# Kernel tuning notes

Hardware: AMD Instinct MI355X
Metric: run time of the kernel (lower is better)

The kernel has to match this reference:

```python
import jax, jax.numpy as jnp
import numpy as np

NV = 10           # int(0.5 // 0.05), clamped to [2, 1000]
STEP = 0.05
HALF_V = 0.5
EPS = 1e-8


def _normalize(x):
    return x / (jnp.linalg.norm(x, axis=-1, keepdims=True) + EPS)


def _bilinear(img, uv):
    # img: [3, H, W]; uv: [N, 2] normalized to [0, 1). align_corners=False convention.
    C, H, W = img.shape
    x = uv[:, 0] * W - 0.5
    y = uv[:, 1] * H - 0.5
    x0 = jnp.floor(x); y0 = jnp.floor(y)
    wx = x - x0; wy = y - y0
    x0i = jnp.clip(x0.astype(jnp.int32), 0, W - 1)
    x1i = jnp.clip(x0i + 1, 0, W - 1)
    y0i = jnp.clip(y0.astype(jnp.int32), 0, H - 1)
    y1i = jnp.clip(y0i + 1, 0, H - 1)
    g = lambda yi, xi: img[:, yi, xi].T  # [N, 3]
    return (g(y0i, x0i) * ((1 - wx) * (1 - wy))[:, None]
            + g(y0i, x1i) * (wx * (1 - wy))[:, None]
            + g(y1i, x0i) * ((1 - wx) * wy)[:, None]
            + g(y1i, x1i) * (wx * wy)[:, None])


def _forward(edge_points, rgb1, rgb2, intrinsic1, intrinsic2, extrinsic1, extrinsic2, nh):
    # nh: concrete numpy int64 [E] of per-edge horizontal sample counts (non-differentiable).
    start = edge_points[:, 0]
    cur_dir = edge_points[:, 1] - start
    next_dir = edge_points[:, 3] - edge_points[:, 1]
    prev_dir = edge_points[:, 0] - edge_points[:, 2]
    cur_length = jnp.linalg.norm(cur_dir + 1e-6, axis=1)
    cur_dir = cur_dir / cur_length[:, None]
    cur_normal = _normalize(jnp.cross(cur_dir, next_dir))
    flip = cur_normal[:, 2] > 0  # dot with (0,0,1) > 0 -> flip sign
    cur_normal = jnp.where(flip[:, None], -cur_normal, cur_normal)
    cur_up = _normalize(jnp.cross(cur_normal, cur_dir))
    prev_normal = _normalize(jnp.cross(prev_dir, cur_dir))

    # ragged per-edge horizontal coordinates via cumsum offsets + repeat_interleave
    begin = np.concatenate([np.zeros(1, np.int64), np.cumsum(nh)[:-1]])
    total_x = int(nh.sum())
    dx = jnp.arange(total_x) - jnp.asarray(np.repeat(begin, nh))
    dx = dx / jnp.asarray(np.repeat(nh - 1, nh)) * jnp.repeat(cur_length, nh, total_repeat_length=total_x)
    dy = jnp.arange(NV) / (NV - 1) * HALF_V  # [NV]
    coords_x = jnp.repeat(dx, NV)            # [total_x * NV]
    coords_y = jnp.tile(dy, total_x)         # [total_x * NV]
    npe = nh * NV
    total = total_x * NV
    pts = (jnp.repeat(cur_dir, npe, axis=0, total_repeat_length=total) * coords_x[:, None]
           + jnp.repeat(cur_up, npe, axis=0, total_repeat_length=total) * coords_y[:, None]
           + jnp.repeat(start, npe, axis=0, total_repeat_length=total))  # [total, 3]

    # project into image 1
    proj1 = pts @ intrinsic1.T
    uv1 = jnp.clip(proj1[:, :2] / proj1[:, 2:3], 0.0, 0.999999)
    s1 = _bilinear(rgb1[0], uv1)

    # project into image 2 via relative transform
    K2h = jnp.eye(4, dtype=pts.dtype).at[:3, :3].set(intrinsic2)
    transform = K2h @ extrinsic2 @ jnp.linalg.inv(extrinsic1)
    pts_h = jnp.concatenate([pts, jnp.ones((pts.shape[0], 1), pts.dtype)], axis=1)
    proj2 = pts_h @ transform.T
    uv2 = jnp.clip(proj2[:, :2] / proj2[:, 2:3], 0.0, 0.999999)
    s2 = _bilinear(rgb2[0], uv2)

    similarity_loss = jnp.mean((s1 - s2) ** 2)
    normal_loss = jnp.mean(1 - jnp.sum(cur_normal * prev_normal, axis=1)) / 2
    observing_normal = _normalize(jnp.cross(edge_points[:, 0], edge_points[:, 1]))
    snp = jnp.minimum(jnp.abs(jnp.sum(cur_up * observing_normal, axis=1)), 0.5)
    normalization_loss = jnp.mean(1 - snp / 0.5)
    return similarity_loss, normal_loss, normalization_loss


def setup_inputs():
    key = jax.random.key(0)
    k0, k1, k2 = jax.random.split(key, 3)
    E = 4000
    ep = jax.random.normal(k0, (E, 4, 3), dtype=jnp.float32) * 1.5
    ep = ep.at[..., 2].add(10.0)  # camera-space points in front of the camera
    rgb1 = jax.random.uniform(k1, (1, 3, 2000, 3000), dtype=jnp.float32)
    rgb2 = jax.random.uniform(k2, (1, 3, 2000, 3000), dtype=jnp.float32)
    K = jnp.array([[0.3, 0.0, 0.5], [0.0, 0.45, 0.5], [0.0, 0.0, 1.0]], jnp.float32)
    E1 = jnp.eye(4, dtype=jnp.float32)
    E2 = jnp.eye(4, dtype=jnp.float32).at[0, 3].set(-0.5)
    return {"edge_points": ep, "rgb1": rgb1, "rgb2": rgb2,
            "intrinsic1": K, "intrinsic2": K, "extrinsic1": E1, "extrinsic2": E2}


def reference(edge_points, rgb1, rgb2, intrinsic1, intrinsic2, extrinsic1, extrinsic2):
    # num_horizontal is an integer count (no gradient in torch either): compute concretely.
    cur_len = np.asarray(jnp.linalg.norm(edge_points[:, 1] - edge_points[:, 0] + 1e-6, axis=1))
    nh = np.clip((cur_len // STEP).astype(np.int64), 2, 1000)
    return _forward(edge_points, rgb1, rgb2, intrinsic1, intrinsic2, extrinsic1, extrinsic2, nh)
```

## Files before the change

### kernel.cpp

```cpp
#include <hip/hip_runtime.h>


constexpr int NVS   = 10;
constexpr int IMG_H = 2000;
constexpr int IMG_W = 3000;
constexpr int NPIX  = IMG_H * IMG_W;
constexpr int SAMPLE_BLOCKS = 2048;
constexpr unsigned CHUNK = 512;

typedef float    fx4 __attribute__((ext_vector_type(4)));
typedef unsigned ux4 __attribute__((ext_vector_type(4)));

struct Geom {
    float p0x, p0y, p0z;
    float p1x, p1y, p1z;
    float p2x, p2y, p2z;
    float p3x, p3y, p3z;
    float cdx, cdy, cdz;
    float cnx, cny, cnz;
    float cux, cuy, cuz;
    float len;
    int   nh;
};

__device__ __forceinline__ Geom compute_geom(const float* __restrict__ ep, int e) {
    Geom g;
    const float* p = ep + (size_t)e * 12;
    g.p0x = p[0];  g.p0y = p[1];  g.p0z = p[2];
    g.p1x = p[3];  g.p1y = p[4];  g.p1z = p[5];
    g.p2x = p[6];  g.p2y = p[7];  g.p2z = p[8];
    g.p3x = p[9];  g.p3y = p[10]; g.p3z = p[11];

    float dx = g.p1x - g.p0x, dy = g.p1y - g.p0y, dz = g.p1z - g.p0z;
    float ax = dx + 1e-6f, ay = dy + 1e-6f, az = dz + 1e-6f;
    g.len = sqrtf(ax * ax + ay * ay + az * az);
    g.cdx = dx / g.len; g.cdy = dy / g.len; g.cdz = dz / g.len;

    float ndx = g.p3x - g.p1x, ndy = g.p3y - g.p1y, ndz = g.p3z - g.p1z;
    float cnx = g.cdy * ndz - g.cdz * ndy;
    float cny = g.cdz * ndx - g.cdx * ndz;
    float cnz = g.cdx * ndy - g.cdy * ndx;
    float n1 = sqrtf(cnx * cnx + cny * cny + cnz * cnz) + 1e-8f;
    cnx /= n1; cny /= n1; cnz /= n1;
    if (cnz > 0.f) { cnx = -cnx; cny = -cny; cnz = -cnz; }
    g.cnx = cnx; g.cny = cny; g.cnz = cnz;

    float cux = cny * g.cdz - cnz * g.cdy;
    float cuy = cnz * g.cdx - cnx * g.cdz;
    float cuz = cnx * g.cdy - cny * g.cdx;
    float n2 = sqrtf(cux * cux + cuy * cuy + cuz * cuz) + 1e-8f;
    g.cux = cux / n2; g.cuy = cuy / n2; g.cuz = cuz / n2;

    int nh = (int)floorf(g.len / 0.05f);
    g.nh = nh < 2 ? 2 : (nh > 1000 ? 1000 : nh);
    return g;
}

__device__ __forceinline__ double block_reduce_d(double v) {
    __shared__ double sh[256];
    int tid = threadIdx.x;
    sh[tid] = v;
    __syncthreads();
    for (int s = 128; s > 0; s >>= 1) {
        if (tid < s) sh[tid] += sh[tid + s];
        __syncthreads();
    }
    double r = sh[0];
    __syncthreads();
    return r;
}

__global__ void setup_kernel(const float* __restrict__ K2,
                             const float* __restrict__ E1,
                             const float* __restrict__ E2,
                             float* __restrict__ tf) {
    if (threadIdx.x != 0 || blockIdx.x != 0) return;

    double a[4][8];
    for (int r = 0; r < 4; ++r)
        for (int c = 0; c < 4; ++c) {
            a[r][c] = (double)E1[r * 4 + c];
            a[r][4 + c] = (r == c) ? 1.0 : 0.0;
        }
    for (int col = 0; col < 4; ++col) {
        int piv = col; double best = fabs(a[col][col]);
        for (int r = col + 1; r < 4; ++r) {
            double t = fabs(a[r][col]);
            if (t > best) { best = t; piv = r; }
        }
        if (piv != col)
            for (int c = 0; c < 8; ++c) { double t = a[col][c]; a[col][c] = a[piv][c]; a[piv][c] = t; }
        double d = a[col][col];
        for (int c = 0; c < 8; ++c) a[col][c] /= d;
        for (int r = 0; r < 4; ++r) {
            if (r == col) continue;
            double f = a[r][col];
            for (int c = 0; c < 8; ++c) a[r][c] -= f * a[col][c];
        }
    }
    double inv1[4][4];
    for (int r = 0; r < 4; ++r)
        for (int c = 0; c < 4; ++c) inv1[r][c] = a[r][4 + c];

    double k2h[4][4];
    for (int r = 0; r < 4; ++r)
        for (int c = 0; c < 4; ++c) k2h[r][c] = (r == c) ? 1.0 : 0.0;
    for (int r = 0; r < 3; ++r)
        for (int c = 0; c < 3; ++c) k2h[r][c] = (double)K2[r * 3 + c];

    double m1[4][4];
    for (int r = 0; r < 4; ++r)
        for (int c = 0; c < 4; ++c) {
            double s = 0.0;
            for (int k = 0; k < 4; ++k) s += (double)E2[r * 4 + k] * inv1[k][c];
            m1[r][c] = s;
        }
    for (int r = 0; r < 4; ++r)
        for (int c = 0; c < 4; ++c) {
            double s = 0.0;
            for (int k = 0; k < 4; ++k) s += k2h[r][k] * m1[k][c];
            tf[r * 4 + c] = (float)s;
        }
}

__global__ __launch_bounds__(256) void edge_kernel(
        const float* __restrict__ ep, int E,
        double* __restrict__ normal_part,
        double* __restrict__ norz_part,
        fx4* __restrict__ geom_out,
        int* __restrict__ nh_out) {
    int e = blockIdx.x * blockDim.x + threadIdx.x;
    double t1 = 0.0, t2 = 0.0;
    if (e < E) {
        Geom g = compute_geom(ep, e);
        float pdx = g.p0x - g.p2x, pdy = g.p0y - g.p2y, pdz = g.p0z - g.p2z;
        float pnx = pdy * g.cdz - pdz * g.cdy;
        float pny = pdz * g.cdx - pdx * g.cdz;
        float pnz = pdx * g.cdy - pdy * g.cdx;
        float n = sqrtf(pnx * pnx + pny * pny + pnz * pnz) + 1e-8f;
        pnx /= n; pny /= n; pnz /= n;
        float dotn = g.cnx * pnx + g.cny * pny + g.cnz * pnz;
        t1 = (double)(1.0f - dotn);

        float ox = g.p0y * g.p1z - g.p0z * g.p1y;
        float oy = g.p0z * g.p1x - g.p0x * g.p1z;
        float oz = g.p0x * g.p1y - g.p0y * g.p1x;
        float no = sqrtf(ox * ox + oy * oy + oz * oz) + 1e-8f;
        ox /= no; oy /= no; oz /= no;
        float snp = fminf(fabsf(g.cux * ox + g.cuy * oy + g.cuz * oz), 0.5f);
        t2 = (double)(1.0f - snp / 0.5f);

        fx4 f0 = {g.cdx, g.cdy, g.cdz, g.len};
        fx4 f1 = {g.cux, g.cuy, g.cuz, 1.0f / (float)(g.nh - 1)};
        fx4 f2 = {g.p0x, g.p0y, g.p0z, 0.f};
        geom_out[e * 3 + 0] = f0;
        geom_out[e * 3 + 1] = f1;
        geom_out[e * 3 + 2] = f2;
        nh_out[e] = g.nh;
    }
    double s1 = block_reduce_d(t1);
    double s2 = block_reduce_d(t2);
    if (threadIdx.x == 0) {
        normal_part[blockIdx.x] = s1;
        norz_part[blockIdx.x]   = s2;
    }
}

__global__ __launch_bounds__(256) void scan_kernel(
        const int* __restrict__ nh, int E, unsigned* __restrict__ cum) {
    __shared__ unsigned ssum[256];
    int tid = threadIdx.x;
    int K = (E + 255) / 256;
    int base = tid * K;

    unsigned s = 0;
    for (int k = 0; k < K; ++k) {
        int idx = base + k;
        if (idx < E) s += (unsigned)(nh[idx] * NVS);
    }
    ssum[tid] = s;
    __syncthreads();
    for (int off = 1; off < 256; off <<= 1) {
        unsigned add = (tid >= off) ? ssum[tid - off] : 0u;
        __syncthreads();
        ssum[tid] += add;
        __syncthreads();
    }
    unsigned run = ssum[tid] - s;
    for (int k = 0; k < K; ++k) {
        int idx = base + k;
        if (idx < E) {
            run += (unsigned)(nh[idx] * NVS);
            cum[idx + 1] = run;
        }
    }
    if (tid == 0) cum[0] = 0;
}

__device__ __forceinline__ unsigned pack_rgb(float r, float g, float b) {
    unsigned ri = (unsigned)__float2int_rn(r * 255.0f) & 255u;
    unsigned gi = (unsigned)__float2int_rn(g * 255.0f) & 255u;
    unsigned bi = (unsigned)__float2int_rn(b * 255.0f) & 255u;
    return ri | (gi << 8) | (bi << 16);
}

__global__ __launch_bounds__(256) void repack_kernel(
        const float* __restrict__ img1, const float* __restrict__ img2,
        unsigned* __restrict__ o1, unsigned* __restrict__ o2) {
    const int nq = NPIX / 4;
    int idx = blockIdx.x * blockDim.x + threadIdx.x;
    if (idx >= 2 * nq) return;
    const float* img;
    unsigned* out;
    int q;
    if (idx < nq) { img = img1; out = o1; q = idx; }
    else          { img = img2; out = o2; q = idx - nq; }

    fx4 r = __builtin_nontemporal_load(reinterpret_cast<const fx4*>(img) + q);
    fx4 g = __builtin_nontemporal_load(reinterpret_cast<const fx4*>(img + NPIX) + q);
    fx4 b = __builtin_nontemporal_load(reinterpret_cast<const fx4*>(img + 2 * (size_t)NPIX) + q);
    ux4 o;
    o.x = pack_rgb(r.x, g.x, b.x);
    o.y = pack_rgb(r.y, g.y, b.y);
    o.z = pack_rgb(r.z, g.z, b.z);
    o.w = pack_rgb(r.w, g.w, b.w);
    reinterpret_cast<ux4*>(out)[q] = o;
}

__device__ __forceinline__ void bilinear3p(const unsigned* __restrict__ img,
                                           float u, float v,
                                           float& r, float& g, float& b) {
    const float INV255 = 1.0f / 255.0f;
    float x = u * (float)IMG_W - 0.5f;
    float y = v * (float)IMG_H - 0.5f;
    float x0 = floorf(x), y0 = floorf(y);
    float wx = x - x0, wy = y - y0;
    int x0i = (int)x0; x0i = x0i < 0 ? 0 : (x0i > IMG_W - 1 ? IMG_W - 1 : x0i);
    int x1i = x0i + 1; x1i = x1i > IMG_W - 1 ? IMG_W - 1 : x1i;
    int y0i = (int)y0; y0i = y0i < 0 ? 0 : (y0i > IMG_H - 1 ? IMG_H - 1 : y0i);
    int y1i = y0i + 1; y1i = y1i > IMG_H - 1 ? IMG_H - 1 : y1i;
    float w00 = (1.f - wx) * (1.f - wy);
    float w10 = wx * (1.f - wy);
    float w01 = (1.f - wx) * wy;
    float w11 = wx * wy;

    unsigned t00 = img[(size_t)y0i * IMG_W + x0i];
    unsigned t10 = img[(size_t)y0i * IMG_W + x1i];
    unsigned t01 = img[(size_t)y1i * IMG_W + x0i];
    unsigned t11 = img[(size_t)y1i * IMG_W + x1i];

    float racc = 0.f, gacc = 0.f, bacc = 0.f;
    auto acc = [&](unsigned t, float w) {
        racc = fmaf(w, (float)(t & 0xffu), racc);
        gacc = fmaf(w, (float)((t >> 8) & 0xffu), gacc);
        bacc = fmaf(w, (float)((t >> 16) & 0xffu), bacc);
    };
    acc(t00, w00); acc(t10, w10); acc(t01, w01); acc(t11, w11);
    r = racc * INV255; g = gacc * INV255; b = bacc * INV255;
}

__device__ __forceinline__ void bilinear3(const float* __restrict__ img,
                                          float u, float v,
                                          float& r, float& g, float& b) {
    float x = u * (float)IMG_W - 0.5f;
    float y = v * (float)IMG_H - 0.5f;
    float x0 = floorf(x), y0 = floorf(y);
    float wx = x - x0, wy = y - y0;
    int x0i = (int)x0; x0i = x0i < 0 ? 0 : (x0i > IMG_W - 1 ? IMG_W - 1 : x0i);
    int x1i = x0i + 1; x1i = x1i > IMG_W - 1 ? IMG_W - 1 : x1i;
    int y0i = (int)y0; y0i = y0i < 0 ? 0 : (y0i > IMG_H - 1 ? IMG_H - 1 : y0i);
    int y1i = y0i + 1; y1i = y1i > IMG_H - 1 ? IMG_H - 1 : y1i;
    float w00 = (1.f - wx) * (1.f - wy);
    float w10 = wx * (1.f - wy);
    float w01 = (1.f - wx) * wy;
    float w11 = wx * wy;
    float out[3];
#pragma unroll
    for (int c = 0; c < 3; ++c) {
        const float* p = img + (size_t)c * NPIX;
        float v00 = p[(size_t)y0i * IMG_W + x0i];
        float v10 = p[(size_t)y0i * IMG_W + x1i];
        float v01 = p[(size_t)y1i * IMG_W + x0i];
        float v11 = p[(size_t)y1i * IMG_W + x1i];
        out[c] = v00 * w00 + v10 * w10 + v01 * w01 + v11 * w11;
    }
    r = out[0]; g = out[1]; b = out[2];
}

__device__ __forceinline__ int find_edge(const unsigned* __restrict__ cum,
                                         int E, unsigned s) {
    int lo = 0, hi = E - 1;
    while (lo < hi) {
        int mid = (lo + hi + 1) >> 1;
        if (cum[mid] <= s) lo = mid; else hi = mid - 1;
    }
    return lo;
}

template <bool PACKED>
__global__ __launch_bounds__(256) void sample_kernel_t(
        const fx4* __restrict__ geom,
        const unsigned* __restrict__ cum, int E,
        const void* __restrict__ img1,
        const void* __restrict__ img2,
        const float* __restrict__ K1,
        const float* __restrict__ tf,
        double* __restrict__ sim_part) {
    __shared__ int sh_ea[2], sh_eb[2];
    int tid = threadIdx.x;

    unsigned NS = cum[E];
    unsigned nch = (NS + CHUNK - 1u) / CHUNK;

    float k00 = K1[0], k01 = K1[1], k02 = K1[2];
    float k10 = K1[3], k11 = K1[4], k12 = K1[5];
    float k20 = K1[6], k21 = K1[7], k22 = K1[8];
    float t00 = tf[0],  t01 = tf[1],  t02 = tf[2],  t03 = tf[3];
    float t10 = tf[4],  t11 = tf[5],  t12 = tf[6],  t13 = tf[7];
    float t20 = tf[8],  t21 = tf[9],  t22 = tf[10], t23 = tf[11];

    double lsum = 0.0;
    int it = 0;

    auto sample_one = [&](unsigned s, int e) {
        while (e + 1 < E && cum[e + 1] <= s) ++e;
        unsigned q = s - cum[e];
        int i = (int)(q / (unsigned)NVS);
        int j = (int)(q - (unsigned)(i * NVS));

        fx4 f0 = geom[e * 3 + 0];
        fx4 f1 = geom[e * 3 + 1];
        fx4 f2 = geom[e * 3 + 2];

        float dxv = ((float)i * f1.w) * f0.w;
        float dyv = ((float)j / 9.0f) * 0.5f;

        float px = f0.x * dxv + f1.x * dyv + f2.x;
        float py = f0.y * dxv + f1.y * dyv + f2.y;
        float pz = f0.z * dxv + f1.z * dyv + f2.z;

        float w1 = k20 * px + k21 * py + k22 * pz;
        float u1 = (k00 * px + k01 * py + k02 * pz) / w1;
        float v1 = (k10 * px + k11 * py + k12 * pz) / w1;
        u1 = fminf(fmaxf(u1, 0.f), 0.999999f);
        v1 = fminf(fmaxf(v1, 0.f), 0.999999f);

        float w2 = t20 * px + t21 * py + t22 * pz + t23;
        float u2 = (t00 * px + t01 * py + t02 * pz + t03) / w2;
        float v2 = (t10 * px + t11 * py + t12 * pz + t13) / w2;
        u2 = fminf(fmaxf(u2, 0.f), 0.999999f);
        v2 = fminf(fmaxf(v2, 0.f), 0.999999f);

        float s1r, s1g, s1b, s2r, s2g, s2b;
        if constexpr (PACKED) {
            bilinear3p((const unsigned*)img1, u1, v1, s1r, s1g, s1b);
            bilinear3p((const unsigned*)img2, u2, v2, s2r, s2g, s2b);
        } else {
            bilinear3((const float*)img1, u1, v1, s1r, s1g, s1b);
            bilinear3((const float*)img2, u2, v2, s2r, s2g, s2b);
        }

        float dr = s1r - s2r, dg = s1g - s2g, db = s1b - s2b;
        lsum += (double)(dr * dr) + (double)(dg * dg) + (double)(db * db);
    };

    for (unsigned chunk = blockIdx.x; chunk < nch; chunk += gridDim.x, ++it) {
        unsigned sbase = chunk * CHUNK;
        int par = it & 1;
        if (tid == 0) {
            sh_ea[par] = find_edge(cum, E, sbase);
            unsigned smid = sbase + 256u;
            sh_eb[par] = find_edge(cum, E, smid < NS ? smid : NS - 1u);
        }
        __syncthreads();
        int ea = sh_ea[par];
        int eb = sh_eb[par];

        unsigned sA = sbase + (unsigned)tid;
        unsigned sB = sA + 256u;
        if (sA < NS) sample_one(sA, ea);
        if (sB < NS) sample_one(sB, eb);
    }

    double tot = block_reduce_d(lsum);
    if (tid == 0) sim_part[blockIdx.x] = tot;
}

__global__ __launch_bounds__(256) void finalize_kernel(
        const double* __restrict__ sim_part, int n_sim,
        const unsigned* __restrict__ cum, int E,
        const double* __restrict__ normal_part,
        const double* __restrict__ norz_part, int n_a,
        float* __restrict__ out) {
    int tid = threadIdx.x;
    unsigned NS = cum[E];

    double s = 0.0;
    for (int i = tid; i < n_sim; i += 256) s += sim_part[i];
    double sim = block_reduce_d(s);

    s = 0.0;
    for (int i = tid; i < n_a; i += 256) s += normal_part[i];
    double nrm = block_reduce_d(s);

    s = 0.0;
    for (int i = tid; i < n_a; i += 256) s += norz_part[i];
    double nz = block_reduce_d(s);

    if (tid == 0) {
        double total = (double)NS * 3.0;
        out[0] = (float)(sim / total);
        out[1] = (float)((nrm / (double)E) * 0.5);
        out[2] = (float)(nz / (double)E);
    }
}

extern "C" void kernel_launch(void* const* d_in, const int* in_sizes, int n_in,
                              void* d_out, int out_size, void* d_ws, size_t ws_size,
                              hipStream_t stream) {
    const float* ep  = (const float*)d_in[0];
    const float* im1 = (const float*)d_in[1];
    const float* im2 = (const float*)d_in[2];
    const float* K1  = (const float*)d_in[3];
    const float* K2  = (const float*)d_in[4];
    const float* E1  = (const float*)d_in[5];
    const float* E2  = (const float*)d_in[6];
    float* out = (float*)d_out;

    int E  = in_sizes[0] / 12;
    int nA = (E + 255) / 256;

    size_t img_bytes = (size_t)NPIX * 4;

    char* ws = (char*)d_ws;
    size_t off = 0;
    auto alloc = [&](size_t bytes) {
        size_t o = off;
        off = (off + bytes + 255) & ~(size_t)255;
        return (void*)(ws + o);
    };

    fx4*      geom        = (fx4*)alloc((size_t)E * 48);
    int*      nh_arr      = (int*)alloc((size_t)E * 4);
    unsigned* cum         = (unsigned*)alloc((size_t)(E + 1) * 4);
    float*    tf          = (float*)alloc(64);
    double*   sim_part    = (double*)alloc((size_t)SAMPLE_BLOCKS * 8);
    double*   normal_part = (double*)alloc((size_t)nA * 8);
    double*   norz_part   = (double*)alloc((size_t)nA * 8);
    size_t tail_bytes = off;

    bool packed = ws_size >= tail_bytes + 2 * img_bytes + 512;
    unsigned* p1 = nullptr;
    unsigned* p2 = nullptr;
    if (packed) {
        p1 = (unsigned*)alloc(img_bytes);
        p2 = (unsigned*)alloc(img_bytes);
    }

    setup_kernel<<<1, 64, 0, stream>>>(K2, E1, E2, tf);
    edge_kernel<<<nA, 256, 0, stream>>>(ep, E, normal_part, norz_part, geom, nh_arr);
    scan_kernel<<<1, 256, 0, stream>>>(nh_arr, E, cum);
    if (packed) {
        const int nq2 = 2 * (NPIX / 4);
        repack_kernel<<<(nq2 + 255) / 256, 256, 0, stream>>>(im1, im2, p1, p2);
        sample_kernel_t<true><<<SAMPLE_BLOCKS, 256, 0, stream>>>(
            geom, cum, E, (const void*)p1, (const void*)p2, K1, tf, sim_part);
    } else {
        sample_kernel_t<false><<<SAMPLE_BLOCKS, 256, 0, stream>>>(
            geom, cum, E, (const void*)im1, (const void*)im2, K1, tf, sim_part);
    }
    finalize_kernel<<<1, 256, 0, stream>>>(sim_part, SAMPLE_BLOCKS, cum, E,
                                           normal_part, norz_part, nA, out);
}
```

Before: 99.01 us.

## Per-wavefront sample units with batched gathers and merged setup/scan kernel

```diff
diff --git a/kernel.cpp b/kernel.cpp
--- a/kernel.cpp
+++ b/kernel.cpp
@@ -6,7 +6,6 @@
 constexpr int IMG_W = 3000;
 constexpr int NPIX  = IMG_H * IMG_W;
 constexpr int SAMPLE_BLOCKS = 2048;
-constexpr unsigned CHUNK = 512;
 
 typedef float    fx4 __attribute__((ext_vector_type(4)));
 typedef unsigned ux4 __attribute__((ext_vector_type(4)));
@@ -68,59 +67,6 @@
     double r = sh[0];
     __syncthreads();
     return r;
-}
-
-__global__ void setup_kernel(const float* __restrict__ K2,
-                             const float* __restrict__ E1,
-                             const float* __restrict__ E2,
-                             float* __restrict__ tf) {
-    if (threadIdx.x != 0 || blockIdx.x != 0) return;
-
-    double a[4][8];
-    for (int r = 0; r < 4; ++r)
-        for (int c = 0; c < 4; ++c) {
-            a[r][c] = (double)E1[r * 4 + c];
-            a[r][4 + c] = (r == c) ? 1.0 : 0.0;
-        }
-    for (int col = 0; col < 4; ++col) {
-        int piv = col; double best = fabs(a[col][col]);
-        for (int r = col + 1; r < 4; ++r) {
-            double t = fabs(a[r][col]);
-            if (t > best) { best = t; piv = r; }
-        }
-        if (piv != col)
-            for (int c = 0; c < 8; ++c) { double t = a[col][c]; a[col][c] = a[piv][c]; a[piv][c] = t; }
-        double d = a[col][col];
-        for (int c = 0; c < 8; ++c) a[col][c] /= d;
-        for (int r = 0; r < 4; ++r) {
-            if (r == col) continue;
-            double f = a[r][col];
-            for (int c = 0; c < 8; ++c) a[r][c] -= f * a[col][c];
-        }
-    }
-    double inv1[4][4];
-    for (int r = 0; r < 4; ++r)
-        for (int c = 0; c < 4; ++c) inv1[r][c] = a[r][4 + c];
-
-    double k2h[4][4];
-    for (int r = 0; r < 4; ++r)
-        for (int c = 0; c < 4; ++c) k2h[r][c] = (r == c) ? 1.0 : 0.0;
-    for (int r = 0; r < 3; ++r)
-        for (int c = 0; c < 3; ++c) k2h[r][c] = (double)K2[r * 3 + c];
-
-    double m1[4][4];
-    for (int r = 0; r < 4; ++r)
-        for (int c = 0; c < 4; ++c) {
-            double s = 0.0;
-            for (int k = 0; k < 4; ++k) s += (double)E2[r * 4 + k] * inv1[k][c];
-            m1[r][c] = s;
-        }
-    for (int r = 0; r < 4; ++r)
-        for (int c = 0; c < 4; ++c) {
-            double s = 0.0;
-            for (int k = 0; k < 4; ++k) s += k2h[r][k] * m1[k][c];
-            tf[r * 4 + c] = (float)s;
-        }
 }
 
 __global__ __launch_bounds__(256) void edge_kernel(
@@ -166,8 +112,10 @@
     }
 }
 
-__global__ __launch_bounds__(256) void scan_kernel(
-        const int* __restrict__ nh, int E, unsigned* __restrict__ cum) {
+__global__ __launch_bounds__(256) void prep_kernel(
+        const int* __restrict__ nh, int E, unsigned* __restrict__ cum,
+        const float* __restrict__ K2, const float* __restrict__ E1,
+        const float* __restrict__ E2, float* __restrict__ tf) {
     __shared__ unsigned ssum[256];
     int tid = threadIdx.x;
     int K = (E + 255) / 256;
@@ -194,7 +142,55 @@
             cum[idx + 1] = run;
         }
     }
-    if (tid == 0) cum[0] = 0;
+    if (tid == 0) {
+        cum[0] = 0;
+
+        double a[4][8];
+        for (int r = 0; r < 4; ++r)
+            for (int c = 0; c < 4; ++c) {
+                a[r][c] = (double)E1[r * 4 + c];
+                a[r][4 + c] = (r == c) ? 1.0 : 0.0;
+            }
+        for (int col = 0; col < 4; ++col) {
+            int piv = col; double best = fabs(a[col][col]);
+            for (int r = col + 1; r < 4; ++r) {
+                double t = fabs(a[r][col]);
+                if (t > best) { best = t; piv = r; }
+            }
+            if (piv != col)
+                for (int c = 0; c < 8; ++c) { double t = a[col][c]; a[col][c] = a[piv][c]; a[piv][c] = t; }
+            double d = a[col][col];
+            for (int c = 0; c < 8; ++c) a[col][c] /= d;
+            for (int r = 0; r < 4; ++r) {
+                if (r == col) continue;
+                double f = a[r][col];
+                for (int c = 0; c < 8; ++c) a[r][c] -= f * a[col][c];
+            }
+        }
+        double inv1[4][4];
+        for (int r = 0; r < 4; ++r)
+            for (int c = 0; c < 4; ++c) inv1[r][c] = a[r][4 + c];
+
+        double k2h[4][4];
+        for (int r = 0; r < 4; ++r)
+            for (int c = 0; c < 4; ++c) k2h[r][c] = (r == c) ? 1.0 : 0.0;
+        for (int r = 0; r < 3; ++r)
+            for (int c = 0; c < 3; ++c) k2h[r][c] = (double)K2[r * 3 + c];
+
+        double m1[4][4];
+        for (int r = 0; r < 4; ++r)
+            for (int c = 0; c < 4; ++c) {
+                double sm = 0.0;
+                for (int k = 0; k < 4; ++k) sm += (double)E2[r * 4 + k] * inv1[k][c];
+                m1[r][c] = sm;
+            }
+        for (int r = 0; r < 4; ++r)
+            for (int c = 0; c < 4; ++c) {
+                double sm = 0.0;
+                for (int k = 0; k < 4; ++k) sm += k2h[r][k] * m1[k][c];
+                tf[r * 4 + c] = (float)sm;
+            }
+    }
 }
 
 __device__ __forceinline__ unsigned pack_rgb(float r, float g, float b) {
@@ -227,10 +223,13 @@
     reinterpret_cast<ux4*>(out)[q] = o;
 }
 
-__device__ __forceinline__ void bilinear3p(const unsigned* __restrict__ img,
-                                           float u, float v,
-                                           float& r, float& g, float& b) {
-    const float INV255 = 1.0f / 255.0f;
+struct BPrep {
+    unsigned i00, i10, i01, i11;
+    float w00, w10, w01, w11;
+};
+
+__device__ __forceinline__ BPrep prep_uv(float u, float v) {
+    BPrep p;
     float x = u * (float)IMG_W - 0.5f;
     float y = v * (float)IMG_H - 0.5f;
     float x0 = floorf(x), y0 = floorf(y);
@@ -239,50 +238,47 @@
     int x1i = x0i + 1; x1i = x1i > IMG_W - 1 ? IMG_W - 1 : x1i;
     int y0i = (int)y0; y0i = y0i < 0 ? 0 : (y0i > IMG_H - 1 ? IMG_H - 1 : y0i);
     int y1i = y0i + 1; y1i = y1i > IMG_H - 1 ? IMG_H - 1 : y1i;
-    float w00 = (1.f - wx) * (1.f - wy);
-    float w10 = wx * (1.f - wy);
-    float w01 = (1.f - wx) * wy;
-    float w11 = wx * wy;
-
-    unsigned t00 = img[(size_t)y0i * IMG_W + x0i];
-    unsigned t10 = img[(size_t)y0i * IMG_W + x1i];
-    unsigned t01 = img[(size_t)y1i * IMG_W + x0i];
-    unsigned t11 = img[(size_t)y1i * IMG_W + x1i];
-
+    p.w00 = (1.f - wx) * (1.f - wy);
+    p.w10 = wx * (1.f - wy);
+    p.w01 = (1.f - wx) * wy;
+    p.w11 = wx * wy;
+    p.i00 = (unsigned)y0i * IMG_W + (unsigned)x0i;
+    p.i10 = (unsigned)y0i * IMG_W + (unsigned)x1i;
+    p.i01 = (unsigned)y1i * IMG_W + (unsigned)x0i;
+    p.i11 = (unsigned)y1i * IMG_W + (unsigned)x1i;
+    return p;
+}
+
+__device__ __forceinline__ void combine_rgba8(unsigned t00, unsigned t10,
+                                              unsigned t01, unsigned t11,
+                                              const BPrep& p,
+                                              float& r, float& g, float& b) {
     float racc = 0.f, gacc = 0.f, bacc = 0.f;
-    auto acc = [&](unsigned t, float w) {
-        racc = fmaf(w, (float)(t & 0xffu), racc);
-        gacc = fmaf(w, (float)((t >> 8) & 0xffu), gacc);
-        bacc = fmaf(w, (float)((t >> 16) & 0xffu), bacc);
-    };
-    acc(t00, w00); acc(t10, w10); acc(t01, w01); acc(t11, w11);
-    r = racc * INV255; g = gacc * INV255; b = bacc * INV255;
+    racc = fmaf(p.w00, (float)(t00 & 0xffu), racc);
+    gacc = fmaf(p.w00, (float)((t00 >> 8) & 0xffu), gacc);
+    bacc = fmaf(p.w00, (float)((t00 >> 16) & 0xffu), bacc);
+    racc = fmaf(p.w10, (float)(t10 & 0xffu), racc);
+    gacc = fmaf(p.w10, (float)((t10 >> 8) & 0xffu), gacc);
+    bacc = fmaf(p.w10, (float)((t10 >> 16) & 0xffu), bacc);
+    racc = fmaf(p.w01, (float)(t01 & 0xffu), racc);
+    gacc = fmaf(p.w01, (float)((t01 >> 8) & 0xffu), gacc);
+    bacc = fmaf(p.w01, (float)((t01 >> 16) & 0xffu), bacc);
+    racc = fmaf(p.w11, (float)(t11 & 0xffu), racc);
+    gacc = fmaf(p.w11, (float)((t11 >> 8) & 0xffu), gacc);
+    bacc = fmaf(p.w11, (float)((t11 >> 16) & 0xffu), bacc);
+    r = racc; g = gacc; b = bacc;
 }
 
 __device__ __forceinline__ void bilinear3(const float* __restrict__ img,
                                           float u, float v,
                                           float& r, float& g, float& b) {
-    float x = u * (float)IMG_W - 0.5f;
-    float y = v * (float)IMG_H - 0.5f;
-    float x0 = floorf(x), y0 = floorf(y);
-    float wx = x - x0, wy = y - y0;
-    int x0i = (int)x0; x0i = x0i < 0 ? 0 : (x0i > IMG_W - 1 ? IMG_W - 1 : x0i);
-    int x1i = x0i + 1; x1i = x1i > IMG_W - 1 ? IMG_W - 1 : x1i;
-    int y0i = (int)y0; y0i = y0i < 0 ? 0 : (y0i > IMG_H - 1 ? IMG_H - 1 : y0i);
-    int y1i = y0i + 1; y1i = y1i > IMG_H - 1 ? IMG_H - 1 : y1i;
-    float w00 = (1.f - wx) * (1.f - wy);
-    float w10 = wx * (1.f - wy);
-    float w01 = (1.f - wx) * wy;
-    float w11 = wx * wy;
+    BPrep p = prep_uv(u, v);
     float out[3];
 #pragma unroll
     for (int c = 0; c < 3; ++c) {
-        const float* p = img + (size_t)c * NPIX;
-        float v00 = p[(size_t)y0i * IMG_W + x0i];
-        float v10 = p[(size_t)y0i * IMG_W + x1i];
-        float v01 = p[(size_t)y1i * IMG_W + x0i];
-        float v11 = p[(size_t)y1i * IMG_W + x1i];
-        out[c] = v00 * w00 + v10 * w10 + v01 * w01 + v11 * w11;
+        const float* pp = img + (size_t)c * NPIX;
+        out[c] = pp[p.i00] * p.w00 + pp[p.i10] * p.w10 +
+                 pp[p.i01] * p.w01 + pp[p.i11] * p.w11;
     }
     r = out[0]; g = out[1]; b = out[2];
 }
@@ -301,16 +297,19 @@
 __global__ __launch_bounds__(256) void sample_kernel_t(
         const fx4* __restrict__ geom,
         const unsigned* __restrict__ cum, int E,
-        const void* __restrict__ img1,
-        const void* __restrict__ img2,
+        const void* __restrict__ vimg1,
+        const void* __restrict__ vimg2,
         const float* __restrict__ K1,
         const float* __restrict__ tf,
         double* __restrict__ sim_part) {
-    __shared__ int sh_ea[2], sh_eb[2];
-    int tid = threadIdx.x;
+    int tid  = threadIdx.x;
+    int lane = tid & 63;
+    int wv   = tid >> 6;
 
     unsigned NS = cum[E];
-    unsigned nch = (NS + CHUNK - 1u) / CHUNK;
+    unsigned nunit = (NS + 383u) / 384u;
+    unsigned wgid = (unsigned)blockIdx.x * 4u + (unsigned)wv;
+    unsigned nw   = (unsigned)gridDim.x * 4u;
 
     float k00 = K1[0], k01 = K1[1], k02 = K1[2];
     float k10 = K1[3], k11 = K1[4], k12 = K1[5];
@@ -319,68 +318,115 @@
     float t10 = tf[4],  t11 = tf[5],  t12 = tf[6],  t13 = tf[7];
     float t20 = tf[8],  t21 = tf[9],  t22 = tf[10], t23 = tf[11];
 
+    const unsigned* img1 = (const unsigned*)vimg1;
+    const unsigned* img2 = (const unsigned*)vimg2;
+    const float* fimg1 = (const float*)vimg1;
+    const float* fimg2 = (const float*)vimg2;
+
     double lsum = 0.0;
-    int it = 0;
-
-    auto sample_one = [&](unsigned s, int e) {
-        while (e + 1 < E && cum[e + 1] <= s) ++e;
+
+    auto project = [&](unsigned s, int e, float& u1, float& v1,
+                       float& u2, float& v2) {
         unsigned q = s - cum[e];
         int i = (int)(q / (unsigned)NVS);
         int j = (int)(q - (unsigned)(i * NVS));
-
         fx4 f0 = geom[e * 3 + 0];
         fx4 f1 = geom[e * 3 + 1];
         fx4 f2 = geom[e * 3 + 2];
-
         float dxv = ((float)i * f1.w) * f0.w;
         float dyv = ((float)j / 9.0f) * 0.5f;
-
         float px = f0.x * dxv + f1.x * dyv + f2.x;
         float py = f0.y * dxv + f1.y * dyv + f2.y;
         float pz = f0.z * dxv + f1.z * dyv + f2.z;
-
         float w1 = k20 * px + k21 * py + k22 * pz;
-        float u1 = (k00 * px + k01 * py + k02 * pz) / w1;
-        float v1 = (k10 * px + k11 * py + k12 * pz) / w1;
+        u1 = (k00 * px + k01 * py + k02 * pz) / w1;
+        v1 = (k10 * px + k11 * py + k12 * pz) / w1;
         u1 = fminf(fmaxf(u1, 0.f), 0.999999f);
         v1 = fminf(fmaxf(v1, 0.f), 0.999999f);
-
         float w2 = t20 * px + t21 * py + t22 * pz + t23;
-        float u2 = (t00 * px + t01 * py + t02 * pz + t03) / w2;
-        float v2 = (t10 * px + t11 * py + t12 * pz + t13) / w2;
+        u2 = (t00 * px + t01 * py + t02 * pz + t03) / w2;
+        v2 = (t10 * px + t11 * py + t12 * pz + t13) / w2;
         u2 = fminf(fmaxf(u2, 0.f), 0.999999f);
         v2 = fminf(fmaxf(v2, 0.f), 0.999999f);
-
-        float s1r, s1g, s1b, s2r, s2g, s2b;
-        if constexpr (PACKED) {
-            bilinear3p((const unsigned*)img1, u1, v1, s1r, s1g, s1b);
-            bilinear3p((const unsigned*)img2, u2, v2, s2r, s2g, s2b);
-        } else {
-            bilinear3((const float*)img1, u1, v1, s1r, s1g, s1b);
-            bilinear3((const float*)img2, u2, v2, s2r, s2g, s2b);
-        }
-
-        float dr = s1r - s2r, dg = s1g - s2g, db = s1b - s2b;
+    };
+
+    auto accum_fp32 = [&](unsigned s, int e) {
+        float u1, v1, u2, v2;
+        project(s, e, u1, v1, u2, v2);
+        float ar, ag, ab, br, bg, bb;
+        bilinear3(fimg1, u1, v1, ar, ag, ab);
+        bilinear3(fimg2, u2, v2, br, bg, bb);
+        float dr = ar - br, dg = ag - bg, db = ab - bb;
         lsum += (double)(dr * dr) + (double)(dg * dg) + (double)(db * db);
     };
 
-    for (unsigned chunk = blockIdx.x; chunk < nch; chunk += gridDim.x, ++it) {
-        unsigned sbase = chunk * CHUNK;
-        int par = it & 1;
-        if (tid == 0) {
-            sh_ea[par] = find_edge(cum, E, sbase);
-            unsigned smid = sbase + 256u;
-            sh_eb[par] = find_edge(cum, E, smid < NS ? smid : NS - 1u);
+    for (unsigned u = wgid; u < nunit; u += nw) {
+        unsigned base = u * 384u + (unsigned)lane;
+        if (base >= NS) continue;
+        int e = find_edge(cum, E, base);
+
+#pragma unroll 1
+        for (int k = 0; k < 6; k += 2) {
+            unsigned sA = base + (unsigned)k * 64u;
+            unsigned sB = sA + 64u;
+            bool okA = sA < NS;
+            bool okB = sB < NS;
+            if (!okA) break;
+
+            if constexpr (PACKED) {
+                while (e + 1 < E && cum[e + 1] <= sA) ++e;
+                float uA1, vA1, uA2, vA2;
+                project(sA, e, uA1, vA1, uA2, vA2);
+                BPrep pA1 = prep_uv(uA1, vA1);
+                BPrep pA2 = prep_uv(uA2, vA2);
+
+                int eB = e;
+                float uB1, vB1, uB2, vB2;
+                BPrep pB1, pB2;
+                if (okB) {
+                    while (eB + 1 < E && cum[eB + 1] <= sB) ++eB;
+                    project(sB, eB, uB1, vB1, uB2, vB2);
+                    pB1 = prep_uv(uB1, vB1);
+                    pB2 = prep_uv(uB2, vB2);
+                } else {
+                    pB1 = pA1; pB2 = pA2;
+                }
+
+                unsigned a00 = img1[pA1.i00], a10 = img1[pA1.i10];
+                unsigned a01 = img1[pA1.i01], a11 = img1[pA1.i11];
+                unsigned c00 = img2[pA2.i00], c10 = img2[pA2.i10];
+                unsigned c01 = img2[pA2.i01], c11 = img2[pA2.i11];
+                unsigned b00 = img1[pB1.i00], b10 = img1[pB1.i10];
+                unsigned b01 = img1[pB1.i01], b11 = img1[pB1.i11];
+                unsigned d00 = img2[pB2.i00], d10 = img2[pB2.i10];
+                unsigned d01 = img2[pB2.i01], d11 = img2[pB2.i11];
+
+                float ar, ag, ab, cr, cg, cb;
+                combine_rgba8(a00, a10, a01, a11, pA1, ar, ag, ab);
+                combine_rgba8(c00, c10, c01, c11, pA2, cr, cg, cb);
+                float dr = ar - cr, dg = ag - cg, db = ab - cb;
+                lsum += (double)(dr * dr) + (double)(dg * dg) + (double)(db * db);
+
+                if (okB) {
+                    float br, bg, bb, er, eg, eb;
+                    combine_rgba8(b00, b10, b01, b11, pB1, br, bg, bb);
+                    combine_rgba8(d00, d10, d01, d11, pB2, er, eg, eb);
+                    float dr2 = br - er, dg2 = bg - eg, db2 = bb - eb;
+                    lsum += (double)(dr2 * dr2) + (double)(dg2 * dg2) + (double)(db2 * db2);
+                    e = eB;
+                }
+            } else {
+                while (e + 1 < E && cum[e + 1] <= sA) ++e;
+                accum_fp32(sA, e);
+                if (okB) {
+                    while (e + 1 < E && cum[e + 1] <= sB) ++e;
+                    accum_fp32(sB, e);
+                }
+            }
         }
-        __syncthreads();
-        int ea = sh_ea[par];
-        int eb = sh_eb[par];
-
-        unsigned sA = sbase + (unsigned)tid;
-        unsigned sB = sA + 256u;
-        if (sA < NS) sample_one(sA, ea);
-        if (sB < NS) sample_one(sB, eb);
-    }
+    }
+
+    if constexpr (PACKED) lsum *= (1.0 / (255.0 * 255.0));
 
     double tot = block_reduce_d(lsum);
     if (tid == 0) sim_part[blockIdx.x] = tot;
@@ -457,9 +503,8 @@
         p2 = (unsigned*)alloc(img_bytes);
     }
 
-    setup_kernel<<<1, 64, 0, stream>>>(K2, E1, E2, tf);
     edge_kernel<<<nA, 256, 0, stream>>>(ep, E, normal_part, norz_part, geom, nh_arr);
-    scan_kernel<<<1, 256, 0, stream>>>(nh_arr, E, cum);
+    prep_kernel<<<1, 256, 0, stream>>>(nh_arr, E, cum, K2, E1, E2, tf);
     if (packed) {
         const int nq2 = 2 * (NPIX / 4);
         repack_kernel<<<(nq2 + 255) / 256, 256, 0, stream>>>(im1, im2, p1, p2);
```

Result: slower. 104.8 us (+5.8%).
